# Kernel tuning notes

Measured on AMD Instinct MI355X. Metric: run time of the kernel, lower is better.

The kernel has to match this reference:

```python
import jax, jax.numpy as jnp
import numpy as np

N_DATA = 12288
N_QUERY = 12288
DIM = 3
RADIUS = 0.085  # gives ~32 neighbors/query for uniform points in [0,1]^3


def setup_inputs() -> dict:
    key = jax.random.key(0)
    k1, k2 = jax.random.split(key)
    data = jax.random.uniform(k1, (N_DATA, DIM), dtype=jnp.float32)
    queries = jax.random.uniform(k2, (N_QUERY, DIM), dtype=jnp.float32)
    radius = jnp.float32(RADIUS)
    return {"data": data, "queries": queries, "radius": radius}


def reference(data, queries, radius):
    # Dense, jit-compatible equivalent of KDTree.query_radius with return_distance=True.
    # Original returns ragged CSR (neighbors_index, neighbors_row_splits, weights=dists**2).
    # Fixed-shape encoding: boolean membership mask [M, N] (row m, col n True iff
    # data[n] is a neighbor of queries[m]; CSR indices = nonzero cols in row order),
    # row_splits [M+1] (exact CSR splits), and dense weights [M, N] = squared
    # distance where within radius else 0 (CSR weights = masked entries in row order).
    sq_d = jnp.sum(data * data, axis=-1)          # [N]
    sq_q = jnp.sum(queries * queries, axis=-1)    # [M]
    # ||q - d||^2 = ||q||^2 + ||d||^2 - 2 q.d  (GEMM form)
    d2 = sq_q[:, None] + sq_d[None, :] - 2.0 * (queries @ data.T)  # [M, N]
    d2 = jnp.maximum(d2, 0.0)
    mask = d2 <= radius * radius                  # [M, N]
    counts = jnp.sum(mask, axis=-1, dtype=jnp.int32)  # [M]
    row_splits = jnp.concatenate(
        [jnp.zeros((1,), jnp.int32), jnp.cumsum(counts)]
    )  # [M+1], matches nbr_dict['neighbors_row_splits']
    weights = jnp.where(mask, d2, 0.0)            # dists**2, masked
    return row_splits, mask, weights
```

## Files before the change

kernel.cpp:

```cpp
#include <hip/hip_runtime.h>


#define TILE 2048

__global__ __launch_bounds__(256) void nbr_kernel(
    const float* __restrict__ data,
    const float* __restrict__ queries,
    const float* __restrict__ radius_p,
    float* __restrict__ out,
    int* __restrict__ counts,
    int N, long long mask_off, long long w_off)
{
    __shared__ float tile[TILE * 3];

    const int m = blockIdx.x;
    const int tid = threadIdx.x;

    const float r = radius_p[0];
    const float r2 = __fmul_rn(r, r);
    const float q0 = queries[3 * m + 0];
    const float q1 = queries[3 * m + 1];
    const float q2 = queries[3 * m + 2];
    const float sq_q = __fadd_rn(
        __fadd_rn(__fmul_rn(q0, q0), __fmul_rn(q1, q1)), __fmul_rn(q2, q2));

    float* mask_row = out + mask_off + (long long)m * N;
    float* w_row    = out + w_off    + (long long)m * N;

    int cnt = 0;

    auto compute = [&](float d0, float d1, float d2e, float& mv, float& wv) -> int {
        const float sq_d = __fadd_rn(
            __fadd_rn(__fmul_rn(d0, d0), __fmul_rn(d1, d1)), __fmul_rn(d2e, d2e));
        const float dot = __fmaf_rn(q2, d2e, __fmaf_rn(q1, d1, __fmul_rn(q0, d0)));
        const float s = __fadd_rn(sq_q, sq_d);
        float v = __fsub_rn(s, __fmul_rn(2.0f, dot));
        v = fmaxf(v, 0.0f);
        const bool in = (v <= r2);
        mv = in ? 1.0f : 0.0f;
        wv = in ? v : 0.0f;
        return in ? 1 : 0;
    };

    for (int tb = 0; tb < N; tb += TILE) {
        const int lim = min(TILE, N - tb);

        __syncthreads();
        if (lim == TILE) {
            const float4* src = reinterpret_cast<const float4*>(data + 3LL * tb);
            float4* dst = reinterpret_cast<float4*>(tile);
            #pragma unroll
            for (int w = 0; w < TILE * 3 / 4 / 256; ++w)
                dst[w * 256 + tid] = src[w * 256 + tid];
        } else {
            for (int w = tid; w < lim * 3; w += 256)
                tile[w] = data[3LL * tb + w];
        }
        __syncthreads();

        if (lim == TILE) {
            #pragma unroll
            for (int k = 0; k < TILE / 256; ++k) {
                const int e = k * 256 + tid;
                const float d0  = tile[3 * e + 0];
                const float d1  = tile[3 * e + 1];
                const float d2e = tile[3 * e + 2];
                float mv, wv;
                cnt += compute(d0, d1, d2e, mv, wv);
                mask_row[tb + e] = mv;
                w_row[tb + e] = wv;
            }
        } else {
            for (int e = tid; e < lim; e += 256) {
                const float d0  = tile[3 * e + 0];
                const float d1  = tile[3 * e + 1];
                const float d2e = tile[3 * e + 2];
                float mv, wv;
                cnt += compute(d0, d1, d2e, mv, wv);
                mask_row[tb + e] = mv;
                w_row[tb + e] = wv;
            }
        }
    }

    for (int off = 32; off > 0; off >>= 1) cnt += __shfl_down(cnt, off);
    __shared__ int lds_cnt;
    if (tid == 0) lds_cnt = 0;
    __syncthreads();
    if ((tid & 63) == 0) atomicAdd(&lds_cnt, cnt);
    __syncthreads();
    if (tid == 0) counts[m] = lds_cnt;
}

__global__ __launch_bounds__(256) void scan_kernel(
    const int* __restrict__ counts, float* __restrict__ out, int M)
{
    __shared__ int sums[256];
    const int t = threadIdx.x;
    const int CH = (M + 255) / 256;
    const int base = t * CH;

    int local[64];
    int s = 0;
    for (int i = 0; i < CH; ++i) {
        const int v = (base + i < M) ? counts[base + i] : 0;
        local[i] = v;
        s += v;
    }
    sums[t] = s;
    __syncthreads();
    for (int off = 1; off < 256; off <<= 1) {
        const int v = (t >= off) ? sums[t - off] : 0;
        __syncthreads();
        sums[t] += v;
        __syncthreads();
    }
    int prefix = sums[t] - s;
    for (int i = 0; i < CH; ++i) {
        if (base + i < M) out[base + i] = (float)prefix;
        prefix += local[i];
    }
    if (t == 255) out[M] = (float)prefix;
}

extern "C" void kernel_launch(void* const* d_in, const int* in_sizes, int n_in,
                              void* d_out, int out_size, void* d_ws, size_t ws_size,
                              hipStream_t stream) {
    const float* data    = (const float*)d_in[0];
    const float* queries = (const float*)d_in[1];
    const float* radius  = (const float*)d_in[2];

    const int N = in_sizes[0] / 3;
    const int M = in_sizes[1] / 3;

    float* out = (float*)d_out;
    int* counts = (int*)d_ws;

    const long long mask_off = (long long)M + 1;
    const long long w_off = mask_off + (long long)M * N;

    nbr_kernel<<<M, 256, 0, stream>>>(data, queries, radius, out, counts,
                                      N, mask_off, w_off);
    scan_kernel<<<1, 256, 0, stream>>>(counts, out, M);
}
```

Before: 1.239 ms.

## Vectorize output stores with float4 by realigning the rows

The output rows begin at offset M+1 floats, so they are misaligned by one float. The kernel now stores most elements with float4 writes: the LDS tile is shifted by 3 floats so that groups of four points line up, and the first 15 points plus the last point of each tile are handled with scalar stores. The tile shrinks to 1024, the subtract becomes an FMA, and a generic fallback kernel covers shapes that don't meet the divisibility conditions. The FMA changes rounding slightly, and only 252 of the 256 threads do vector work in each tile.

```diff
diff --git a/kernel.cpp b/kernel.cpp
--- a/kernel.cpp
+++ b/kernel.cpp
@@ -1,7 +1,7 @@
 #include <hip/hip_runtime.h>
 
 
-#define TILE 2048
+#define TILE 1024
 
 __global__ __launch_bounds__(256) void nbr_kernel(
     const float* __restrict__ data,
@@ -11,7 +11,7 @@
     int* __restrict__ counts,
     int N, long long mask_off, long long w_off)
 {
-    __shared__ float tile[TILE * 3];
+    __shared__ __align__(16) float tile[TILE * 3 + 4];
 
     const int m = blockIdx.x;
     const int tid = threadIdx.x;
@@ -34,7 +34,7 @@
             __fadd_rn(__fmul_rn(d0, d0), __fmul_rn(d1, d1)), __fmul_rn(d2e, d2e));
         const float dot = __fmaf_rn(q2, d2e, __fmaf_rn(q1, d1, __fmul_rn(q0, d0)));
         const float s = __fadd_rn(sq_q, sq_d);
-        float v = __fsub_rn(s, __fmul_rn(2.0f, dot));
+        float v = __fmaf_rn(-2.0f, dot, s);
         v = fmaxf(v, 0.0f);
         const bool in = (v <= r2);
         mv = in ? 1.0f : 0.0f;
@@ -42,47 +42,88 @@
         return in ? 1 : 0;
     };
 
+    constexpr int NQ = (TILE - 16) / 4;
+
     for (int tb = 0; tb < N; tb += TILE) {
-        const int lim = min(TILE, N - tb);
-
         __syncthreads();
-        if (lim == TILE) {
+        {
             const float4* src = reinterpret_cast<const float4*>(data + 3LL * tb);
-            float4* dst = reinterpret_cast<float4*>(tile);
             #pragma unroll
-            for (int w = 0; w < TILE * 3 / 4 / 256; ++w)
-                dst[w * 256 + tid] = src[w * 256 + tid];
-        } else {
-            for (int w = tid; w < lim * 3; w += 256)
-                tile[w] = data[3LL * tb + w];
+            for (int k = 0; k < 3 * TILE / 4 / 256; ++k) {
+                const int f = k * 256 + tid;
+                const float4 v = src[f];
+                const int w = 4 * f + 3;
+                tile[w + 0] = v.x;
+                tile[w + 1] = v.y;
+                tile[w + 2] = v.z;
+                tile[w + 3] = v.w;
+            }
         }
         __syncthreads();
 
-        if (lim == TILE) {
-            #pragma unroll
-            for (int k = 0; k < TILE / 256; ++k) {
-                const int e = k * 256 + tid;
-                const float d0  = tile[3 * e + 0];
-                const float d1  = tile[3 * e + 1];
-                const float d2e = tile[3 * e + 2];
-                float mv, wv;
-                cnt += compute(d0, d1, d2e, mv, wv);
-                mask_row[tb + e] = mv;
-                w_row[tb + e] = wv;
-            }
-        } else {
-            for (int e = tid; e < lim; e += 256) {
-                const float d0  = tile[3 * e + 0];
-                const float d1  = tile[3 * e + 1];
-                const float d2e = tile[3 * e + 2];
-                float mv, wv;
-                cnt += compute(d0, d1, d2e, mv, wv);
-                mask_row[tb + e] = mv;
-                w_row[tb + e] = wv;
-            }
+        if (tid < 16) {
+            const int n = (tid < 15) ? tid : (TILE - 1);
+            float mv, wv;
+            cnt += compute(tile[3 * n + 3], tile[3 * n + 4], tile[3 * n + 5], mv, wv);
+            mask_row[tb + n] = mv;
+            w_row[tb + n] = wv;
+        }
+
+        if (tid < NQ) {
+            const int c = tid;
+            const float4 A = *reinterpret_cast<const float4*>(&tile[48 + 12 * c]);
+            const float4 B = *reinterpret_cast<const float4*>(&tile[52 + 12 * c]);
+            const float4 C = *reinterpret_cast<const float4*>(&tile[56 + 12 * c]);
+            float4 mv, wv;
+            cnt += compute(A.x, A.y, A.z, mv.x, wv.x);
+            cnt += compute(A.w, B.x, B.y, mv.y, wv.y);
+            cnt += compute(B.z, B.w, C.x, mv.z, wv.z);
+            cnt += compute(C.y, C.z, C.w, mv.w, wv.w);
+            const long long g = (long long)tb + 15 + 4 * c;
+            *reinterpret_cast<float4*>(mask_row + g) = mv;
+            *reinterpret_cast<float4*>(w_row + g) = wv;
         }
     }
 
+    for (int off = 32; off > 0; off >>= 1) cnt += __shfl_down(cnt, off);
+    __shared__ int lds_cnt;
+    if (tid == 0) lds_cnt = 0;
+    __syncthreads();
+    if ((tid & 63) == 0) atomicAdd(&lds_cnt, cnt);
+    __syncthreads();
+    if (tid == 0) counts[m] = lds_cnt;
+}
+
+__global__ __launch_bounds__(256) void nbr_kernel_generic(
+    const float* __restrict__ data,
+    const float* __restrict__ queries,
+    const float* __restrict__ radius_p,
+    float* __restrict__ out,
+    int* __restrict__ counts,
+    int N, long long mask_off, long long w_off)
+{
+    const int m = blockIdx.x;
+    const int tid = threadIdx.x;
+    const float r = radius_p[0];
+    const float r2 = __fmul_rn(r, r);
+    const float q0 = queries[3 * m + 0], q1 = queries[3 * m + 1], q2 = queries[3 * m + 2];
+    const float sq_q = __fadd_rn(
+        __fadd_rn(__fmul_rn(q0, q0), __fmul_rn(q1, q1)), __fmul_rn(q2, q2));
+    float* mask_row = out + mask_off + (long long)m * N;
+    float* w_row    = out + w_off    + (long long)m * N;
+    int cnt = 0;
+    for (int n = tid; n < N; n += 256) {
+        const float d0 = data[3 * n], d1 = data[3 * n + 1], d2e = data[3 * n + 2];
+        const float sq_d = __fadd_rn(
+            __fadd_rn(__fmul_rn(d0, d0), __fmul_rn(d1, d1)), __fmul_rn(d2e, d2e));
+        const float dot = __fmaf_rn(q2, d2e, __fmaf_rn(q1, d1, __fmul_rn(q0, d0)));
+        float v = __fmaf_rn(-2.0f, dot, __fadd_rn(sq_q, sq_d));
+        v = fmaxf(v, 0.0f);
+        const bool in = (v <= r2);
+        mask_row[n] = in ? 1.0f : 0.0f;
+        w_row[n] = in ? v : 0.0f;
+        cnt += in ? 1 : 0;
+    }
     for (int off = 32; off > 0; off >>= 1) cnt += __shfl_down(cnt, off);
     __shared__ int lds_cnt;
     if (tid == 0) lds_cnt = 0;
@@ -139,7 +180,13 @@
     const long long mask_off = (long long)M + 1;
     const long long w_off = mask_off + (long long)M * N;
 
-    nbr_kernel<<<M, 256, 0, stream>>>(data, queries, radius, out, counts,
-                                      N, mask_off, w_off);
+    const bool fast = (N % TILE == 0) && (M % 16 == 0) && (N % 16 == 0);
+    if (fast) {
+        nbr_kernel<<<M, 256, 0, stream>>>(data, queries, radius, out, counts,
+                                          N, mask_off, w_off);
+    } else {
+        nbr_kernel_generic<<<M, 256, 0, stream>>>(data, queries, radius, out,
+                                                  counts, N, mask_off, w_off);
+    }
     scan_kernel<<<1, 256, 0, stream>>>(counts, out, M);
 }
```

New measurement: 1.259 ms. About the same (+1.6%).
